# Optimization experiments

Hardware: AMD Instinct MI355X
Metric: run time of the kernel (lower is better)

## Reference

```python
import jax, jax.numpy as jnp
import numpy as np

N = 100000
E = 3200000
K = 4
BN_EPS = 1e-5


def spmm(edge_rows, edge_cols, edge_vals, x):
    # y = A @ x with A in COO: y[r] += v * x[c]
    msgs = edge_vals[:, None] * x[edge_cols]           # [E, d]
    return jax.ops.segment_sum(msgs, edge_rows, num_segments=N)


def setup_inputs() -> dict:
    key = jax.random.key(0)
    ks = jax.random.split(key, 8)
    d_in, d_h, d_out = 256, 256, 64
    return {
        "x": jax.random.normal(ks[0], (N, d_in), jnp.float32),
        "edge_rows": jax.random.randint(ks[1], (E,), 0, N, jnp.int32),
        "edge_cols": jax.random.randint(ks[2], (E,), 0, N, jnp.int32),
        "edge_vals": jax.random.uniform(ks[3], (E,), jnp.float32),
        "bn_gamma": jnp.ones((d_in,), jnp.float32),
        "bn_beta": jnp.zeros((d_in,), jnp.float32),
        "w_in": jax.random.normal(ks[4], (d_in, d_h), jnp.float32) * 0.05,
        "b_in": jnp.zeros((d_h,), jnp.float32),
        "w_conv": jax.random.normal(ks[5], (d_h, d_h), jnp.float32) * 0.05,
        "b_conv": jnp.zeros((d_h,), jnp.float32),
        "w_out": jax.random.normal(ks[6], (d_h, d_out), jnp.float32) * 0.05,
        "b_out": jnp.zeros((d_out,), jnp.float32),
    }


def reference(x, edge_rows, edge_cols, edge_vals, bn_gamma, bn_beta,
              w_in, b_in, w_conv, b_conv, w_out, b_out):
    # BatchNorm1d over node dimension (training-mode batch stats, biased var)
    mean = jnp.mean(x, axis=0)
    var = jnp.var(x, axis=0)
    x = (x - mean) * jax.lax.rsqrt(var + BN_EPS) * bn_gamma + bn_beta
    # in_conv + tanh
    x = jnp.tanh(x @ w_in + b_in)
    # SGConv: k spmm hops then linear, then tanh
    for _ in range(K):
        x = spmm(edge_rows, edge_cols, edge_vals, x)
    x = jnp.tanh(x @ w_conv + b_conv)
    # out_conv (logits)
    return x @ w_out + b_out
```

## Files before the change

kernel.cpp:

```cpp
#include <hip/hip_runtime.h>
#include <hip/hip_fp16.h>

#define NN   100000
#define NNP  100096
#define EE   3200000
#define DD   256
#define DOUTC 64
#define LSTR 40

typedef _Float16 half8 __attribute__((ext_vector_type(8)));
typedef _Float16 half4 __attribute__((ext_vector_type(4)));
typedef float    f32x4 __attribute__((ext_vector_type(4)));

__device__ inline f32x4 mfma16(half8 a, half8 b, f32x4 c) {
    return __builtin_amdgcn_mfma_f32_16x16x32_f16(a, b, c, 0, 0, 0);
}

__global__ void col_stats_kernel(const float* __restrict__ x, float* __restrict__ stats) {
    int t = threadIdx.x;
    int r0 = blockIdx.x * 256;
    int r1 = min(r0 + 256, NN);
    float s = 0.f, s2 = 0.f;
    for (int r = r0; r < r1; ++r) {
        float v = x[(size_t)r * DD + t];
        s += v; s2 += v * v;
    }
    atomicAdd(&stats[t], s);
    atomicAdd(&stats[DD + t], s2);
}

__global__ void fold_bias_kernel(const float* __restrict__ stats,
                                 const float* __restrict__ gamma,
                                 const float* __restrict__ beta,
                                 const float* __restrict__ w_in,
                                 const float* __restrict__ b_in,
                                 float* __restrict__ bfold) {
    __shared__ float sb[DD];
    int t = threadIdx.x;
    float mean = stats[t] * (1.0f / NN);
    float var  = stats[DD + t] * (1.0f / NN) - mean * mean;
    float a = gamma[t] * rsqrtf(var + 1e-5f);
    sb[t] = beta[t] - mean * a;
    __syncthreads();
    float acc = 0.f;
    for (int j = 0; j < DD; ++j) acc += sb[j] * w_in[j * DD + t];
    bfold[t] = b_in[t] + acc;
}

__global__ void split_w1_kernel(const float* __restrict__ stats,
                                const float* __restrict__ gamma,
                                const float* __restrict__ w_in,
                                _Float16* __restrict__ wth, _Float16* __restrict__ wtl) {
    int k = blockIdx.x, n = threadIdx.x;
    float mean = stats[k] * (1.0f / NN);
    float var  = stats[DD + k] * (1.0f / NN) - mean * mean;
    float a = gamma[k] * rsqrtf(var + 1e-5f);
    float v = a * w_in[(size_t)k * DD + n];
    _Float16 hi = (_Float16)v;
    _Float16 lo = (_Float16)(v - (float)hi);
    wth[(size_t)n * DD + k] = hi;
    wtl[(size_t)n * DD + k] = lo;
}

__global__ void split_w_kernel(const float* __restrict__ w, int ncols,
                               _Float16* __restrict__ wth, _Float16* __restrict__ wtl) {
    int k = blockIdx.x, n = threadIdx.x;
    float v = w[(size_t)k * ncols + n];
    _Float16 hi = (_Float16)v;
    _Float16 lo = (_Float16)(v - (float)hi);
    wth[(size_t)n * DD + k] = hi;
    wtl[(size_t)n * DD + k] = lo;
}

__global__ void hist_kernel(const int* __restrict__ rows, int* __restrict__ cnt,
                            int* __restrict__ rank) {
    int e = blockIdx.x * blockDim.x + threadIdx.x;
    if (e < EE) rank[e] = atomicAdd(&cnt[rows[e]], 1);
}

__global__ void scan1_kernel(const int* __restrict__ in, int* __restrict__ out,
                             int* __restrict__ bsums, int n) {
    __shared__ int s[256];
    int t = threadIdx.x;
    int base = blockIdx.x * 1024;
    int v[4]; int local = 0;
    for (int i = 0; i < 4; ++i) {
        int idx = base + t * 4 + i;
        v[i] = (idx < n) ? in[idx] : 0;
        local += v[i];
    }
    s[t] = local;
    __syncthreads();
    for (int off = 1; off < 256; off <<= 1) {
        int xv = 0;
        if (t >= off) xv = s[t - off];
        __syncthreads();
        if (t >= off) s[t] += xv;
        __syncthreads();
    }
    int excl = s[t] - local;
    if (t == 255) bsums[blockIdx.x] = s[255];
    int run = excl;
    for (int i = 0; i < 4; ++i) {
        int idx = base + t * 4 + i;
        if (idx < n) out[idx] = run;
        run += v[i];
    }
}

__global__ void scan2_kernel(int* __restrict__ bsums, int nb) {
    __shared__ int s[256];
    int t = threadIdx.x;
    int v = (t < nb) ? bsums[t] : 0;
    s[t] = v;
    __syncthreads();
    for (int off = 1; off < 256; off <<= 1) {
        int xv = 0;
        if (t >= off) xv = s[t - off];
        __syncthreads();
        if (t >= off) s[t] += xv;
        __syncthreads();
    }
    if (t < nb) bsums[t] = s[t] - v;
}

__global__ void scan3_kernel(int* __restrict__ out, const int* __restrict__ bsums, int n) {
    int t = threadIdx.x;
    int base = blockIdx.x * 1024;
    int add = bsums[blockIdx.x];
    for (int i = 0; i < 4; ++i) {
        int idx = base + t * 4 + i;
        if (idx < n) out[idx] += add;
    }
    if (blockIdx.x == 0 && t == 0) out[n] = EE;
}

__global__ void scatter_kernel(const int* __restrict__ rows, const int* __restrict__ cols,
                               const float* __restrict__ vals, const int* __restrict__ rp,
                               const int* __restrict__ rank, int2* __restrict__ edges) {
    int e = blockIdx.x * blockDim.x + threadIdx.x;
    if (e >= EE) return;
    int r = __builtin_nontemporal_load(&rows[e]);
    int c = __builtin_nontemporal_load(&cols[e]);
    float v = __builtin_nontemporal_load(&vals[e]);
    int rk = __builtin_nontemporal_load(&rank[e]);
    int pos = rp[r] + rk;
    edges[pos] = make_int2(c, __float_as_int(v));
}

__global__ __launch_bounds__(256) void spmm_kernel(
        const int* __restrict__ rp, const int2* __restrict__ edges,
        const __half* __restrict__ xin, __half* __restrict__ xout, int ph) {
    int tid = threadIdx.x;
    int lane = tid & 63;
    int sub = lane >> 4;
    int sl = lane & 15;
    int r = __builtin_amdgcn_readfirstlane(blockIdx.x * 4 + (tid >> 6));
    int e0 = rp[r], e1 = rp[r + 1];
    const float4* xi = (const float4*)xin;
    const long long* epk = (const long long*)edges;
    int cbase = ph * 16 + sl;

    float acc[8] = {0.f,0.f,0.f,0.f,0.f,0.f,0.f,0.f};

    int base = e0;
    for (; base + 8 <= e1; base += 8) {
        long long p0 = __builtin_nontemporal_load(&epk[base + sub]);
        long long p1 = __builtin_nontemporal_load(&epk[base + 4 + sub]);
        int c0 = (int)(unsigned int)p0, c1 = (int)(unsigned int)p1;
        float v0 = __int_as_float((int)(p0 >> 32));
        float v1 = __int_as_float((int)(p1 >> 32));
        float4 x0 = xi[(size_t)c0 * 32 + cbase];
        float4 x1 = xi[(size_t)c1 * 32 + cbase];
        {
            const __half2* hp = (const __half2*)&x0;
            float2 f0 = __half22float2(hp[0]);
            float2 f1 = __half22float2(hp[1]);
            float2 f2 = __half22float2(hp[2]);
            float2 f3 = __half22float2(hp[3]);
            acc[0] += v0*f0.x; acc[1] += v0*f0.y;
            acc[2] += v0*f1.x; acc[3] += v0*f1.y;
            acc[4] += v0*f2.x; acc[5] += v0*f2.y;
            acc[6] += v0*f3.x; acc[7] += v0*f3.y;
        }
        {
            const __half2* hp = (const __half2*)&x1;
            float2 f0 = __half22float2(hp[0]);
            float2 f1 = __half22float2(hp[1]);
            float2 f2 = __half22float2(hp[2]);
            float2 f3 = __half22float2(hp[3]);
            acc[0] += v1*f0.x; acc[1] += v1*f0.y;
            acc[2] += v1*f1.x; acc[3] += v1*f1.y;
            acc[4] += v1*f2.x; acc[5] += v1*f2.y;
            acc[6] += v1*f3.x; acc[7] += v1*f3.y;
        }
    }
    if (base < e1) {
#pragma unroll
        for (int i = 0; i < 2; ++i) {
            int idx = base + 4*i + sub;
            bool valid = idx < e1;
            int idxc = valid ? idx : e0;
            long long p = epk[idxc];
            int c = (int)(unsigned int)p;
            float v = valid ? __int_as_float((int)(p >> 32)) : 0.f;
            float4 xv = xi[(size_t)c * 32 + cbase];
            const __half2* hp = (const __half2*)&xv;
            float2 f0 = __half22float2(hp[0]);
            float2 f1 = __half22float2(hp[1]);
            float2 f2 = __half22float2(hp[2]);
            float2 f3 = __half22float2(hp[3]);
            acc[0] += v*f0.x; acc[1] += v*f0.y;
            acc[2] += v*f1.x; acc[3] += v*f1.y;
            acc[4] += v*f2.x; acc[5] += v*f2.y;
            acc[6] += v*f3.x; acc[7] += v*f3.y;
        }
    }
#pragma unroll
    for (int j = 0; j < 8; ++j) {
        acc[j] += __shfl_xor(acc[j], 16, 64);
        acc[j] += __shfl_xor(acc[j], 32, 64);
    }
    if (sub == 0) {
        union { __half h[8]; f32x4 f; } u;
#pragma unroll
        for (int j = 0; j < 8; ++j) u.h[j] = __float2half_rn(acc[j]);
        __builtin_nontemporal_store(u.f, (f32x4*)&((float4*)xout)[(size_t)r * 32 + cbase]);
    }
}

template<bool SPLIT_A, bool TANH, typename Tout, int BN>
__global__ __launch_bounds__(256) void gemm_mfma(
    const void* __restrict__ Av, const _Float16* __restrict__ WTh,
    const _Float16* __restrict__ WTl, const float* __restrict__ bias,
    Tout* __restrict__ C, int M_A, int M_C, int NC)
{
    __shared__ _Float16 As_hi[128 * LSTR];
    __shared__ _Float16 As_lo[(SPLIT_A ? 128 : 1) * LSTR];
    __shared__ _Float16 Ws_hi[BN * LSTR];
    __shared__ _Float16 Ws_lo[BN * LSTR];

    int tid = threadIdx.x;
    int lane = tid & 63;
    int w = tid >> 6;
    int q = lane >> 4;
    int r16 = lane & 15;
    int m0 = blockIdx.x * 128;
    int n0 = blockIdx.y * BN;

    constexpr int MT = (BN == 128) ? 4 : 2;
    int wm = (BN == 128) ? (w & 1) * 64 : w * 32;
    int wn = (BN == 128) ? (w >> 1) * 64 : 0;

    f32x4 acc[MT][4];
#pragma unroll
    for (int mt = 0; mt < MT; ++mt)
#pragma unroll
        for (int nt = 0; nt < 4; ++nt) acc[mt][nt] = (f32x4){0.f, 0.f, 0.f, 0.f};

    for (int k0 = 0; k0 < 256; k0 += 32) {
        if (SPLIT_A) {
            const float* A = (const float*)Av;
#pragma unroll
            for (int p = 0; p < 4; ++p) {
                int idx = tid + p * 256;
                int m = idx >> 3, kc = idx & 7;
                int gm = m0 + m;
                float4 av = make_float4(0.f, 0.f, 0.f, 0.f);
                if (gm < M_A) av = *(const float4*)&A[(size_t)gm * 256 + k0 + kc * 4];
                half4 hi, lo;
                hi.x = (_Float16)av.x; lo.x = (_Float16)(av.x - (float)hi.x);
                hi.y = (_Float16)av.y; lo.y = (_Float16)(av.y - (float)hi.y);
                hi.z = (_Float16)av.z; lo.z = (_Float16)(av.z - (float)hi.z);
                hi.w = (_Float16)av.w; lo.w = (_Float16)(av.w - (float)hi.w);
                *(half4*)&As_hi[m * LSTR + kc * 4] = hi;
                *(half4*)&As_lo[m * LSTR + kc * 4] = lo;
            }
        } else {
            const _Float16* A = (const _Float16*)Av;
#pragma unroll
            for (int p = 0; p < 2; ++p) {
                int idx = tid + p * 256;
                int m = idx >> 2, kc = idx & 3;
                half8 av = *(const half8*)&A[(size_t)(m0 + m) * 256 + k0 + kc * 8];
                *(half8*)&As_hi[m * LSTR + kc * 8] = av;
            }
        }
#pragma unroll
        for (int p = 0; p < BN / 64; ++p) {
            int idx = tid + p * 256;
            int n = idx >> 2, kc = idx & 3;
            *(half8*)&Ws_hi[n * LSTR + kc * 8] = *(const half8*)&WTh[(size_t)(n0 + n) * 256 + k0 + kc * 8];
            *(half8*)&Ws_lo[n * LSTR + kc * 8] = *(const half8*)&WTl[(size_t)(n0 + n) * 256 + k0 + kc * 8];
        }
        __syncthreads();

        half8 af_h[MT], af_l[MT], wf_h[4], wf_l[4];
#pragma unroll
        for (int mt = 0; mt < MT; ++mt) {
            int mrow = wm + mt * 16 + r16;
            af_h[mt] = *(const half8*)&As_hi[mrow * LSTR + q * 8];
            if (SPLIT_A) af_l[mt] = *(const half8*)&As_lo[mrow * LSTR + q * 8];
        }
#pragma unroll
        for (int nt = 0; nt < 4; ++nt) {
            int nrow = wn + nt * 16 + r16;
            wf_h[nt] = *(const half8*)&Ws_hi[nrow * LSTR + q * 8];
            wf_l[nt] = *(const half8*)&Ws_lo[nrow * LSTR + q * 8];
        }
#pragma unroll
        for (int mt = 0; mt < MT; ++mt)
#pragma unroll
            for (int nt = 0; nt < 4; ++nt) {
                acc[mt][nt] = mfma16(af_h[mt], wf_h[nt], acc[mt][nt]);
                if (SPLIT_A) acc[mt][nt] = mfma16(af_l[mt], wf_h[nt], acc[mt][nt]);
                acc[mt][nt] = mfma16(af_h[mt], wf_l[nt], acc[mt][nt]);
            }
        __syncthreads();
    }

#pragma unroll
    for (int nt = 0; nt < 4; ++nt) {
        float b = bias[n0 + wn + nt * 16 + r16];
        int gc = n0 + wn + nt * 16 + r16;
#pragma unroll
        for (int mt = 0; mt < MT; ++mt) {
#pragma unroll
            for (int r = 0; r < 4; ++r) {
                int gm = m0 + wm + mt * 16 + q * 4 + r;
                float v = acc[mt][nt][r] + b;
                if (TANH) v = tanhf(v);
                if (gm < M_C) C[(size_t)gm * NC + gc] = (Tout)v;
            }
        }
    }
}

extern "C" void kernel_launch(void* const* d_in, const int* in_sizes, int n_in,
                              void* d_out, int out_size, void* d_ws, size_t ws_size,
                              hipStream_t stream) {
    const float* x      = (const float*)d_in[0];
    const int*   erows  = (const int*)d_in[1];
    const int*   ecols  = (const int*)d_in[2];
    const float* evals  = (const float*)d_in[3];
    const float* gamma  = (const float*)d_in[4];
    const float* beta   = (const float*)d_in[5];
    const float* w_in   = (const float*)d_in[6];
    const float* b_in   = (const float*)d_in[7];
    const float* w_conv = (const float*)d_in[8];
    const float* b_conv = (const float*)d_in[9];
    const float* w_out  = (const float*)d_in[10];
    const float* b_out  = (const float*)d_in[11];
    float* out = (float*)d_out;

    char* ws = (char*)d_ws;
    size_t off = 0;
    auto alloc = [&](size_t bytes) -> void* {
        void* p = ws + off;
        off = (off + bytes + 255) & ~(size_t)255;
        return p;
    };
    _Float16* h1   = (_Float16*)alloc((size_t)NNP * DD * 2);
    _Float16* h2   = (_Float16*)alloc((size_t)NNP * DD * 2);
    int2*  edges = (int2*) alloc((size_t)EE * 8);
    int*   rank  = (int*)  alloc((size_t)EE * 4);
    int*   rp    = (int*)  alloc((size_t)(NN + 1) * 4);
    int*   cnt   = (int*)  alloc((size_t)NN * 4);
    float* stats = (float*)alloc(2 * DD * 4);
    int*   bsums = (int*)  alloc(128 * 4);
    _Float16* wt1h = (_Float16*)alloc((size_t)DD * DD * 2);
    _Float16* wt1l = (_Float16*)alloc((size_t)DD * DD * 2);
    _Float16* wt2h = (_Float16*)alloc((size_t)DD * DD * 2);
    _Float16* wt2l = (_Float16*)alloc((size_t)DD * DD * 2);
    _Float16* wt3h = (_Float16*)alloc((size_t)DOUTC * DD * 2);
    _Float16* wt3l = (_Float16*)alloc((size_t)DOUTC * DD * 2);
    float* bfold = (float*)alloc(DD * 4);

    hipMemsetAsync(cnt,   0, (size_t)NN * 4, stream);
    hipMemsetAsync(stats, 0, 2 * DD * 4, stream);

    hist_kernel<<<(EE + 255) / 256, 256, 0, stream>>>(erows, cnt, rank);
    int nb = (NN + 1023) / 1024;
    scan1_kernel<<<nb, 256, 0, stream>>>(cnt, rp, bsums, NN);
    scan2_kernel<<<1, 256, 0, stream>>>(bsums, nb);
    scan3_kernel<<<nb, 256, 0, stream>>>(rp, bsums, NN);
    scatter_kernel<<<(EE + 255) / 256, 256, 0, stream>>>(erows, ecols, evals, rp, rank, edges);

    col_stats_kernel<<<(NN + 255) / 256, 256, 0, stream>>>(x, stats);
    fold_bias_kernel<<<1, 256, 0, stream>>>(stats, gamma, beta, w_in, b_in, bfold);
    split_w1_kernel<<<DD, DD, 0, stream>>>(stats, gamma, w_in, wt1h, wt1l);
    split_w_kernel<<<DD, DD, 0, stream>>>(w_conv, DD, wt2h, wt2l);
    split_w_kernel<<<DD, DOUTC, 0, stream>>>(w_out, DOUTC, wt3h, wt3l);

    dim3 g2(NNP / 128, 2), g1(NNP / 128, 1);
    gemm_mfma<true, true, _Float16, 128><<<g2, 256, 0, stream>>>(
        x, wt1h, wt1l, bfold, h1, NN, NNP, DD);

    spmm_kernel<<<NN / 4, 256, 0, stream>>>(rp, edges, (const __half*)h1, (__half*)h2, 0);
    spmm_kernel<<<NN / 4, 256, 0, stream>>>(rp, edges, (const __half*)h1, (__half*)h2, 1);
    spmm_kernel<<<NN / 4, 256, 0, stream>>>(rp, edges, (const __half*)h2, (__half*)h1, 0);
    spmm_kernel<<<NN / 4, 256, 0, stream>>>(rp, edges, (const __half*)h2, (__half*)h1, 1);
    spmm_kernel<<<NN / 4, 256, 0, stream>>>(rp, edges, (const __half*)h1, (__half*)h2, 0);
    spmm_kernel<<<NN / 4, 256, 0, stream>>>(rp, edges, (const __half*)h1, (__half*)h2, 1);
    spmm_kernel<<<NN / 4, 256, 0, stream>>>(rp, edges, (const __half*)h2, (__half*)h1, 0);
    spmm_kernel<<<NN / 4, 256, 0, stream>>>(rp, edges, (const __half*)h2, (__half*)h1, 1);

    gemm_mfma<false, true, _Float16, 128><<<g2, 256, 0, stream>>>(
        h1, wt2h, wt2l, b_conv, h2, NNP, NNP, DD);
    gemm_mfma<false, false, float, 64><<<g1, 256, 0, stream>>>(
        h2, wt3h, wt3l, b_out, out, NNP, NN, DOUTC);
}
```

Before: 1.634 ms.

## Replace global-atomic COO-to-CSR conversion with two-pass bucketed LDS sort

Converts COO to CSR with a two-level bucket sort. Edges are first counted and scattered into 128-row buckets using per-block shared-memory histograms and a column-wise prefix scan. Each bucket is then sorted locally by row in LDS, and row offsets are written out. This replaces the per-edge global atomicAdd histogram and its random scatter, which contend heavily, at the cost of an extra 8-byte-per-edge intermediate buffer and more kernel launches.

```diff
diff --git a/kernel.cpp b/kernel.cpp
--- a/kernel.cpp
+++ b/kernel.cpp
@@ -7,6 +7,10 @@
 #define DD   256
 #define DOUTC 64
 #define LSTR 40
+
+#define NBK  782
+#define PB   512
+#define CHUNK 6250
 
 typedef _Float16 half8 __attribute__((ext_vector_type(8)));
 typedef _Float16 half4 __attribute__((ext_vector_type(4)));
@@ -72,23 +76,29 @@
     wtl[(size_t)n * DD + k] = lo;
 }
 
-__global__ void hist_kernel(const int* __restrict__ rows, int* __restrict__ cnt,
-                            int* __restrict__ rank) {
-    int e = blockIdx.x * blockDim.x + threadIdx.x;
-    if (e < EE) rank[e] = atomicAdd(&cnt[rows[e]], 1);
-}
-
-__global__ void scan1_kernel(const int* __restrict__ in, int* __restrict__ out,
-                             int* __restrict__ bsums, int n) {
+__global__ __launch_bounds__(256) void bucket_count_kernel(
+        const int* __restrict__ rows, int* __restrict__ Cm) {
+    __shared__ int bins[NBK];
+    int t = threadIdx.x;
+    for (int i = t; i < NBK; i += 256) bins[i] = 0;
+    __syncthreads();
+    int base = blockIdx.x * CHUNK;
+    for (int e = base + t; e < base + CHUNK; e += 256) {
+        int r = __builtin_nontemporal_load(&rows[e]);
+        atomicAdd(&bins[r >> 7], 1);
+    }
+    __syncthreads();
+    for (int i = t; i < NBK; i += 256) Cm[(size_t)blockIdx.x * NBK + i] = bins[i];
+}
+
+__global__ __launch_bounds__(256) void scan_col_kernel(int* __restrict__ Cm,
+                                                       int* __restrict__ Tb) {
     __shared__ int s[256];
-    int t = threadIdx.x;
-    int base = blockIdx.x * 1024;
-    int v[4]; int local = 0;
-    for (int i = 0; i < 4; ++i) {
-        int idx = base + t * 4 + i;
-        v[i] = (idx < n) ? in[idx] : 0;
-        local += v[i];
-    }
+    int b = blockIdx.x;
+    int t = threadIdx.x;
+    int v0 = Cm[(size_t)(2 * t)     * NBK + b];
+    int v1 = Cm[(size_t)(2 * t + 1) * NBK + b];
+    int local = v0 + v1;
     s[t] = local;
     __syncthreads();
     for (int off = 1; off < 256; off <<= 1) {
@@ -99,20 +109,22 @@
         __syncthreads();
     }
     int excl = s[t] - local;
-    if (t == 255) bsums[blockIdx.x] = s[255];
-    int run = excl;
+    Cm[(size_t)(2 * t)     * NBK + b] = excl;
+    Cm[(size_t)(2 * t + 1) * NBK + b] = excl + v0;
+    if (t == 255) Tb[b] = s[255];
+}
+
+__global__ __launch_bounds__(256) void scan_buckets_kernel(const int* __restrict__ Tb,
+                                                           int* __restrict__ Bb) {
+    __shared__ int s[256];
+    int t = threadIdx.x;
+    int v[4]; int local = 0;
     for (int i = 0; i < 4; ++i) {
-        int idx = base + t * 4 + i;
-        if (idx < n) out[idx] = run;
-        run += v[i];
-    }
-}
-
-__global__ void scan2_kernel(int* __restrict__ bsums, int nb) {
-    __shared__ int s[256];
-    int t = threadIdx.x;
-    int v = (t < nb) ? bsums[t] : 0;
-    s[t] = v;
+        int idx = t * 4 + i;
+        v[i] = (idx < NBK) ? Tb[idx] : 0;
+        local += v[i];
+    }
+    s[t] = local;
     __syncthreads();
     for (int off = 1; off < 256; off <<= 1) {
         int xv = 0;
@@ -121,31 +133,73 @@
         if (t >= off) s[t] += xv;
         __syncthreads();
     }
-    if (t < nb) bsums[t] = s[t] - v;
-}
-
-__global__ void scan3_kernel(int* __restrict__ out, const int* __restrict__ bsums, int n) {
-    int t = threadIdx.x;
-    int base = blockIdx.x * 1024;
-    int add = bsums[blockIdx.x];
+    int excl = s[t] - local;
+    int run = excl;
     for (int i = 0; i < 4; ++i) {
-        int idx = base + t * 4 + i;
-        if (idx < n) out[idx] += add;
-    }
-    if (blockIdx.x == 0 && t == 0) out[n] = EE;
-}
-
-__global__ void scatter_kernel(const int* __restrict__ rows, const int* __restrict__ cols,
-                               const float* __restrict__ vals, const int* __restrict__ rp,
-                               const int* __restrict__ rank, int2* __restrict__ edges) {
-    int e = blockIdx.x * blockDim.x + threadIdx.x;
-    if (e >= EE) return;
-    int r = __builtin_nontemporal_load(&rows[e]);
-    int c = __builtin_nontemporal_load(&cols[e]);
-    float v = __builtin_nontemporal_load(&vals[e]);
-    int rk = __builtin_nontemporal_load(&rank[e]);
-    int pos = rp[r] + rk;
-    edges[pos] = make_int2(c, __float_as_int(v));
+        int idx = t * 4 + i;
+        if (idx < NBK) Bb[idx] = run;
+        run += v[i];
+    }
+    if (t == 255) Bb[NBK] = EE;
+}
+
+__global__ __launch_bounds__(256) void bucket_scatter_kernel(
+        const int* __restrict__ rows, const int* __restrict__ cols,
+        const float* __restrict__ vals, const int* __restrict__ Cm,
+        const int* __restrict__ Bb, int2* __restrict__ ebuf) {
+    __shared__ int bins[NBK];
+    int t = threadIdx.x;
+    for (int i = t; i < NBK; i += 256) bins[i] = 0;
+    __syncthreads();
+    int base = blockIdx.x * CHUNK;
+    for (int e = base + t; e < base + CHUNK; e += 256) {
+        int r = __builtin_nontemporal_load(&rows[e]);
+        int c = __builtin_nontemporal_load(&cols[e]);
+        float v = __builtin_nontemporal_load(&vals[e]);
+        int bkt = r >> 7;
+        int lr = atomicAdd(&bins[bkt], 1);
+        int pos = Bb[bkt] + Cm[(size_t)blockIdx.x * NBK + bkt] + lr;
+        ebuf[pos] = make_int2(c | ((r & 127) << 17), __float_as_int(v));
+    }
+}
+
+__global__ __launch_bounds__(256) void bucket_finalize_kernel(
+        const int* __restrict__ Bb, const int2* __restrict__ ebuf,
+        int* __restrict__ rp, int2* __restrict__ edges) {
+    __shared__ int hist[128];
+    __shared__ int excl[128];
+    __shared__ int cur[128];
+    __shared__ int sc[128];
+    int b = blockIdx.x;
+    int t = threadIdx.x;
+    int e0 = Bb[b], e1 = Bb[b + 1];
+    if (t < 128) { hist[t] = 0; cur[t] = 0; }
+    __syncthreads();
+    for (int e = e0 + t; e < e1; e += 256)
+        atomicAdd(&hist[ebuf[e].x >> 17], 1);
+    __syncthreads();
+    if (t < 128) sc[t] = hist[t];
+    __syncthreads();
+    for (int off = 1; off < 128; off <<= 1) {
+        int xv = 0;
+        if (t < 128 && t >= off) xv = sc[t - off];
+        __syncthreads();
+        if (t < 128 && t >= off) sc[t] += xv;
+        __syncthreads();
+    }
+    if (t < 128) {
+        excl[t] = sc[t] - hist[t];
+        int gr = b * 128 + t;
+        if (gr < NN) rp[gr] = e0 + excl[t];
+    }
+    if (b == 0 && t == 0) rp[NN] = EE;
+    __syncthreads();
+    for (int e = e0 + t; e < e1; e += 256) {
+        int2 d = ebuf[e];
+        int rl = d.x >> 17;
+        int lr = atomicAdd(&cur[rl], 1);
+        edges[e0 + excl[rl] + lr] = make_int2(d.x & 0x1FFFF, d.y);
+    }
 }
 
 __global__ __launch_bounds__(256) void spmm_kernel(
@@ -363,11 +417,12 @@
     _Float16* h1   = (_Float16*)alloc((size_t)NNP * DD * 2);
     _Float16* h2   = (_Float16*)alloc((size_t)NNP * DD * 2);
     int2*  edges = (int2*) alloc((size_t)EE * 8);
-    int*   rank  = (int*)  alloc((size_t)EE * 4);
+    int2*  ebuf  = (int2*) alloc((size_t)EE * 8);
+    int*   Cm    = (int*)  alloc((size_t)PB * NBK * 4);
+    int*   Tb    = (int*)  alloc((size_t)NBK * 4);
+    int*   Bb    = (int*)  alloc((size_t)(NBK + 1) * 4);
     int*   rp    = (int*)  alloc((size_t)(NN + 1) * 4);
-    int*   cnt   = (int*)  alloc((size_t)NN * 4);
     float* stats = (float*)alloc(2 * DD * 4);
-    int*   bsums = (int*)  alloc(128 * 4);
     _Float16* wt1h = (_Float16*)alloc((size_t)DD * DD * 2);
     _Float16* wt1l = (_Float16*)alloc((size_t)DD * DD * 2);
     _Float16* wt2h = (_Float16*)alloc((size_t)DD * DD * 2);
@@ -376,15 +431,13 @@
     _Float16* wt3l = (_Float16*)alloc((size_t)DOUTC * DD * 2);
     float* bfold = (float*)alloc(DD * 4);
 
-    hipMemsetAsync(cnt,   0, (size_t)NN * 4, stream);
     hipMemsetAsync(stats, 0, 2 * DD * 4, stream);
 
-    hist_kernel<<<(EE + 255) / 256, 256, 0, stream>>>(erows, cnt, rank);
-    int nb = (NN + 1023) / 1024;
-    scan1_kernel<<<nb, 256, 0, stream>>>(cnt, rp, bsums, NN);
-    scan2_kernel<<<1, 256, 0, stream>>>(bsums, nb);
-    scan3_kernel<<<nb, 256, 0, stream>>>(rp, bsums, NN);
-    scatter_kernel<<<(EE + 255) / 256, 256, 0, stream>>>(erows, ecols, evals, rp, rank, edges);
+    bucket_count_kernel<<<PB, 256, 0, stream>>>(erows, Cm);
+    scan_col_kernel<<<NBK, 256, 0, stream>>>(Cm, Tb);
+    scan_buckets_kernel<<<1, 256, 0, stream>>>(Tb, Bb);
+    bucket_scatter_kernel<<<PB, 256, 0, stream>>>(erows, ecols, evals, Cm, Bb, ebuf);
+    bucket_finalize_kernel<<<NBK, 256, 0, stream>>>(Bb, ebuf, rp, edges);
 
     col_stats_kernel<<<(NN + 255) / 256, 256, 0, stream>>>(x, stats);
     fold_bias_kernel<<<1, 256, 0, stream>>>(stats, gamma, beta, w_in, b_in, bfold);
```

Result: faster. 1.541 ms (-5.7%).
